# Optimization experiments

Hardware: AMD Instinct MI355X
Metric: run time of the kernel (lower is better)

Reference implementation:

```python
import jax, jax.numpy as jnp
import numpy as np

EPS = 1e-5

def _layernorm(x, gamma):
    # LayerNorm over last dim, no bias (torch LayerNorm(bias=False))
    mu = jnp.mean(x, axis=-1, keepdims=True)
    var = jnp.mean(jnp.square(x - mu), axis=-1, keepdims=True)
    return (x - mu) * jax.lax.rsqrt(var + EPS) * gamma

def setup_inputs() -> dict:
    B, N, D = 32, 1024, 512
    key = jax.random.key(0)
    ks = jax.random.split(key, 6)
    x = jax.random.normal(ks[0], (B, N, D), dtype=jnp.float32)
    # valid lengths in [1, N] so no query row has all keys masked
    belief_base_sizes = jax.random.randint(ks[1], (B,), 1, N + 1, dtype=jnp.int32)
    s = 0.02
    w_qkv = jax.random.normal(ks[2], (D, 3 * D), dtype=jnp.float32) * s
    w_fc = jax.random.normal(ks[3], (D, D), dtype=jnp.float32) * s
    w_proj = jax.random.normal(ks[4], (D, D), dtype=jnp.float32) * s
    g1 = jnp.ones((D,), dtype=jnp.float32)
    g2 = jnp.ones((D,), dtype=jnp.float32)
    return {"x": x, "belief_base_sizes": belief_base_sizes, "g1": g1,
            "w_qkv": w_qkv, "g2": g2, "w_fc": w_fc, "w_proj": w_proj}

def reference(x, belief_base_sizes, g1, w_qkv, g2, w_fc, w_proj):
    B, N, D = x.shape
    h = _layernorm(x, g1)                      # LN1
    qkv = jnp.einsum('bnd,de->bne', h, w_qkv)  # [B,N,3D]
    q, k, v = jnp.split(qkv, 3, axis=-1)
    scores = jnp.einsum('bqd,bkd->bqk', q, k) / jnp.sqrt(jnp.float32(D))
    # mask key columns >= valid size (rows are NOT masked, matching the original)
    col = jnp.arange(N)
    pad = col[None, None, :] >= belief_base_sizes[:, None, None]  # [B,1,N]
    scores = jnp.where(pad, -jnp.inf, scores)
    attn = jax.nn.softmax(scores, axis=-1)
    y = jnp.einsum('bqk,bkd->bqd', attn, v)
    y = _layernorm(y, g2)                      # LN2 (no residual in original)
    y = jnp.einsum('bnd,de->bne', y, w_fc)
    y = jax.nn.gelu(y, approximate=False)      # torch GELU default = exact erf
    y = jnp.einsum('bnd,de->bne', y, w_proj)
    return y
```

## Files before the change

kernel.cpp:

```cpp
#include <hip/hip_runtime.h>
#include <hip/hip_bf16.h>
#include <cmath>


using f16 = _Float16;
typedef _Float16 f16x8 __attribute__((ext_vector_type(8)));
typedef _Float16 f16x4 __attribute__((ext_vector_type(4)));
typedef _Float16 f16x2 __attribute__((ext_vector_type(2)));
typedef float f32x4 __attribute__((ext_vector_type(4)));

#define NB 32
#define NN 1024
#define ND 512

#define GLOAD_LDS16(g, l)                                                     \
    __builtin_amdgcn_global_load_lds(                                         \
        (const __attribute__((address_space(1))) void*)(g),                   \
        (__attribute__((address_space(3))) void*)(l), 16, 0, 0)

__global__ void transpose_cast_all(const float* __restrict__ wqkv, f16* __restrict__ wqkvT,
                                   const float* __restrict__ wfc, f16* __restrict__ wfcT,
                                   const float* __restrict__ wproj, f16* __restrict__ wprojT) {
    const int z = blockIdx.z;
    const float* w = (z == 0) ? wqkv : (z == 1) ? wfc : wproj;
    f16* wT       = (z == 0) ? wqkvT : (z == 1) ? wfcT : wprojT;
    const int Ncols = (z == 0) ? 1536 : 512;
    if ((int)blockIdx.x * 32 >= Ncols) return;

    __shared__ float tile[32][33];
    const int n0 = blockIdx.x * 32, k0 = blockIdx.y * 32;
    const int tx = threadIdx.x, ty = threadIdx.y;
    for (int i = ty; i < 32; i += 8)
        tile[i][tx] = w[(long long)(k0 + i) * Ncols + n0 + tx];
    __syncthreads();
    for (int i = ty; i < 32; i += 8)
        wT[(long long)(n0 + i) * 512 + k0 + tx] = (f16)tile[tx][i];
}

template <typename TIN>
__global__ __launch_bounds__(256) void ln_kernel(const TIN* __restrict__ x,
                                                 const float* __restrict__ gamma,
                                                 f16* __restrict__ out) {
    const int tid = threadIdx.x;
    const long long base = (long long)blockIdx.x * ND;
    float v0, v1;
    if constexpr (sizeof(TIN) == 4) {
        const float2 t = ((const float2*)(x + base))[tid];
        v0 = t.x; v1 = t.y;
    } else {
        const f16x2 t = ((const f16x2*)(x + base))[tid];
        v0 = (float)t.x; v1 = (float)t.y;
    }

    __shared__ float red[8];
    const int wave = tid >> 6, lane = tid & 63;

    float s = v0 + v1;
#pragma unroll
    for (int o = 32; o > 0; o >>= 1) s += __shfl_down(s, o, 64);
    if (lane == 0) red[wave] = s;
    __syncthreads();
    const float mean = (red[0] + red[1] + red[2] + red[3]) * (1.f / 512.f);
    __syncthreads();

    const float d0 = v0 - mean, d1 = v1 - mean;
    float q = d0 * d0 + d1 * d1;
#pragma unroll
    for (int o = 32; o > 0; o >>= 1) q += __shfl_down(q, o, 64);
    if (lane == 0) red[wave] = q;
    __syncthreads();
    const float var = (red[0] + red[1] + red[2] + red[3]) * (1.f / 512.f);
    const float rstd = rsqrtf(var + 1e-5f);

    f16x2 o2;
    o2.x = (f16)(d0 * rstd * gamma[2 * tid]);
    o2.y = (f16)(d1 * rstd * gamma[2 * tid + 1]);
    ((f16x2*)(out + base))[tid] = o2;
}

__global__ __launch_bounds__(256) void softmax_wave(f16* __restrict__ scores,
                                                    const int* __restrict__ sizes) {
    const int b = blockIdx.y;
    const int wave = threadIdx.x >> 6, lane = threadIdx.x & 63;
    const int row = blockIdx.x * 4 + wave;
    f16* srow = scores + ((long long)b * NN + row) * NN;
    const int sz = sizes[b];
    const int keff = (sz + 63) & ~63;
    const int cbase = lane * 16;

    const f16x8 a0 = *(const f16x8*)&srow[cbase];
    const f16x8 a1 = *(const f16x8*)&srow[cbase + 8];
    float v[16];
#pragma unroll
    for (int e = 0; e < 8; e++) { v[e] = (float)a0[e]; v[8 + e] = (float)a1[e]; }

    float m = -1e30f;
#pragma unroll
    for (int e = 0; e < 16; e++)
        if (cbase + e < sz) m = fmaxf(m, v[e]);
#pragma unroll
    for (int o = 32; o > 0; o >>= 1) m = fmaxf(m, __shfl_xor(m, o, 64));

    float s = 0.f;
#pragma unroll
    for (int e = 0; e < 16; e++) {
        v[e] = (cbase + e < sz) ? __expf(v[e] - m) : 0.f;
        s += v[e];
    }
#pragma unroll
    for (int o = 32; o > 0; o >>= 1) s += __shfl_xor(s, o, 64);
    const float inv = 1.f / s;

    if (cbase < keff) {
        f16x8 o0, o1;
#pragma unroll
        for (int e = 0; e < 8; e++) {
            o0[e] = (f16)(v[e] * inv);
            o1[e] = (f16)(v[8 + e] * inv);
        }
        *(f16x8*)&srow[cbase] = o0;
        *(f16x8*)&srow[cbase + 8] = o1;
    }
}

__device__ __forceinline__ float gelu_exact(float x) {
    return 0.5f * x * (1.f + erff(x * 0.70710678118654752f));
}

template <int MODE, int MASKN, int MASKK>
__global__ __launch_bounds__(256) void gemm_bt(
    const f16* __restrict__ A, int lda, long long strideA,
    const f16* __restrict__ Bt, int ldb, long long strideB,
    void* __restrict__ Cv, int ldc, long long strideC,
    int K, float alpha, const int* __restrict__ sizes, void* __restrict__ Cv2) {
    __shared__ __align__(16) f16 As[128 * 64];
    __shared__ __align__(16) f16 Bs[128 * 64];

    const int tid = threadIdx.x;
    const int wave = tid >> 6, lane = tid & 63;
    const int wr = (wave >> 1) * 64, wc = (wave & 1) * 64;
    const int lrow = lane & 15, quad = lane >> 4;
    const long long m0 = (long long)blockIdx.y * 128;
    const long long n0 = (long long)blockIdx.x * 128;

    if (MASKN) {
        if (n0 >= sizes[blockIdx.z]) return;
    }
    int Keff = K;
    if (MASKK) {
        const int ke = (sizes[blockIdx.z] + 63) & ~63;
        if (ke < Keff) Keff = ke;
    }

    A += (long long)blockIdx.z * strideA;
    Bt += (long long)blockIdx.z * strideB;

    f32x4 acc[4][4];
#pragma unroll
    for (int i = 0; i < 4; i++)
#pragma unroll
        for (int j = 0; j < 4; j++) acc[i][j] = (f32x4){0.f, 0.f, 0.f, 0.f};

    const f16* Ap[4];
    const f16* Bp[4];
#pragma unroll
    for (int p = 0; p < 4; p++) {
        const int s = tid + p * 256;
        const int r = s >> 3, c = ((s & 7) ^ (r & 7)) * 8;
        Ap[p] = A + (m0 + r) * lda + c;
        Bp[p] = Bt + (n0 + r) * ldb + c;
    }

    for (int k0 = 0; k0 < Keff; k0 += 64) {
        __syncthreads();
#pragma unroll
        for (int p = 0; p < 4; p++) GLOAD_LDS16(Ap[p] + k0, &As[(tid + p * 256) * 8]);
#pragma unroll
        for (int p = 0; p < 4; p++) GLOAD_LDS16(Bp[p] + k0, &Bs[(tid + p * 256) * 8]);
        __syncthreads();

#pragma unroll
        for (int h = 0; h < 2; h++) {
            const int gq = ((h * 4 + quad) ^ (lrow & 7)) * 8;
            f16x8 af[4], bf[4];
#pragma unroll
            for (int i = 0; i < 4; i++)
                af[i] = *(const f16x8*)&As[(wr + i * 16 + lrow) * 64 + gq];
#pragma unroll
            for (int j = 0; j < 4; j++)
                bf[j] = *(const f16x8*)&Bs[(wc + j * 16 + lrow) * 64 + gq];
#pragma unroll
            for (int i = 0; i < 4; i++)
#pragma unroll
                for (int j = 0; j < 4; j++)
                    acc[i][j] = __builtin_amdgcn_mfma_f32_16x16x32_f16(af[i], bf[j], acc[i][j], 0, 0, 0);
        }
    }

    if (MODE == 3 && n0 >= 1024) {
        f16* vTp = (f16*)Cv2;
#pragma unroll
        for (int i = 0; i < 4; i++) {
            const long long rbase = m0 + wr + i * 16 + quad * 4;
            const long long bb = rbase >> 10;
            const long long nrow = rbase & 1023;
#pragma unroll
            for (int j = 0; j < 4; j++) {
                const long long col = n0 + wc + j * 16 + lrow - 1024;
                f16x4 pk;
#pragma unroll
                for (int r = 0; r < 4; r++) pk[r] = (f16)acc[i][j][r];
                *(f16x4*)&vTp[bb * ND * NN + col * NN + nrow] = pk;
            }
        }
        return;
    }
    float* Cf = (float*)Cv + (long long)blockIdx.z * strideC;
    f16* Ch = (f16*)Cv + (long long)blockIdx.z * strideC;
#pragma unroll
    for (int i = 0; i < 4; i++) {
        const long long rbase = m0 + wr + i * 16 + quad * 4;
#pragma unroll
        for (int j = 0; j < 4; j++) {
            const long long col = n0 + wc + j * 16 + lrow;
#pragma unroll
            for (int r = 0; r < 4; r++) {
                float vv = acc[i][j][r];
                if (MODE == 1) {
                    Cf[(rbase + r) * ldc + col] = vv * alpha;
                } else if (MODE == 2) {
                    Ch[(rbase + r) * ldc + col] = (f16)gelu_exact(vv);
                } else {
                    Ch[(rbase + r) * ldc + col] = (f16)(vv * alpha);
                }
            }
        }
    }
}

extern "C" void kernel_launch(void* const* d_in, const int* in_sizes, int n_in,
                              void* d_out, int out_size, void* d_ws, size_t ws_size,
                              hipStream_t stream) {
    const float* x     = (const float*)d_in[0];
    const int*   sizes = (const int*)d_in[1];
    const float* g1    = (const float*)d_in[2];
    const float* wqkv  = (const float*)d_in[3];
    const float* g2    = (const float*)d_in[4];
    const float* wfc   = (const float*)d_in[5];
    const float* wproj = (const float*)d_in[6];
    float* out = (float*)d_out;
    char* ws = (char*)d_ws;

    f16* wqkvT  = (f16*)(ws + (0ull << 20));
    f16* wfcT   = (f16*)(ws + (2ull << 20));
    f16* wprojT = (f16*)(ws + (3ull << 20));
    f16* qk     = (f16*)(ws + (4ull << 20));
    f16* vT     = (f16*)(ws + (68ull << 20));
    f16* scoresB = (f16*)(ws + (4ull << 20));
    f16* ln2o   = (f16*)(ws + (36ull << 20));
    f16* gelub  = (f16*)(ws + (4ull << 20));

    f16* h       = (f16*)d_out;
    f16* scoresA = (f16*)d_out;
    f16* y       = (f16*)d_out + (long long)NB * NN * ND;

    const long long sstr = (long long)NN * NN;
    const long long qstr = (long long)NN * 1024;
    const long long vstr = (long long)ND * NN;
    const long long ystr = (long long)NN * ND;

    transpose_cast_all<<<dim3(48, 16, 3), dim3(32, 8), 0, stream>>>(
        wqkv, wqkvT, wfc, wfcT, wproj, wprojT);

    ln_kernel<float><<<NB * NN, 256, 0, stream>>>(x, g1, h);

    gemm_bt<3, 0, 0><<<dim3(12, 256, 1), 256, 0, stream>>>(
        h, 512, 0, wqkvT, 512, 0, qk, 1024, 0, 512, 1.0f, nullptr, vT);

    for (int ph = 0; ph < 2; ph++) {
        const int b0 = ph * 16;
        f16* sc = ph ? scoresB : scoresA;
        const f16* qc = qk + (long long)b0 * qstr;

        gemm_bt<0, 1, 0><<<dim3(8, 8, 16), 256, 0, stream>>>(
            qc, 1024, qstr, qc + 512, 1024, qstr,
            sc, NN, sstr, 512, 0.044194173824159216f, sizes + b0, nullptr);

        softmax_wave<<<dim3(NN / 4, 16), 256, 0, stream>>>(sc, sizes + b0);

        gemm_bt<0, 0, 1><<<dim3(4, 8, 16), 256, 0, stream>>>(
            sc, NN, sstr, vT + (long long)b0 * vstr, NN, vstr,
            y + (long long)b0 * ystr, ND, ystr, NN, 1.0f, sizes + b0, nullptr);
    }

    ln_kernel<f16><<<NB * NN, 256, 0, stream>>>(y, g2, ln2o);

    gemm_bt<2, 0, 0><<<dim3(4, 256, 1), 256, 0, stream>>>(
        ln2o, 512, 0, wfcT, 512, 0, gelub, 512, 0, 512, 1.0f, nullptr, nullptr);

    gemm_bt<1, 0, 0><<<dim3(4, 256, 1), 256, 0, stream>>>(
        gelub, 512, 0, wprojT, 512, 0, out, 512, 0, 512, 1.0f, nullptr, nullptr);
}
```

Measured before the change: 438.7 us.

## Merge attention phases into single launches, add XCD-aware tile remap, skip masked softmax loads

Buffers are relocated so the full-batch score matrix fits in the output buffer and y lives in the workspace. That lets the two half-batch attention phases collapse into one QK GEMM, one softmax and one PV GEMM over all 32 batches, cutting kernel launches and tail effects. Non-batched GEMMs remap block IDs so consecutive tiles land on the same XCD, aiming at better L2 reuse on MI355X. Softmax rows skip loading fp16 scores past the padded valid length. The buffer aliasing relies on qk no longer being needed once y is written over its start, and on vT being finished before gelub reuses its space.

```diff
diff --git a/kernel.cpp b/kernel.cpp
--- a/kernel.cpp
+++ b/kernel.cpp
@@ -88,11 +88,16 @@
     const int keff = (sz + 63) & ~63;
     const int cbase = lane * 16;
 
-    const f16x8 a0 = *(const f16x8*)&srow[cbase];
-    const f16x8 a1 = *(const f16x8*)&srow[cbase + 8];
     float v[16];
-#pragma unroll
-    for (int e = 0; e < 8; e++) { v[e] = (float)a0[e]; v[8 + e] = (float)a1[e]; }
+    if (cbase < keff) {
+        const f16x8 a0 = *(const f16x8*)&srow[cbase];
+        const f16x8 a1 = *(const f16x8*)&srow[cbase + 8];
+#pragma unroll
+        for (int e = 0; e < 8; e++) { v[e] = (float)a0[e]; v[8 + e] = (float)a1[e]; }
+    } else {
+#pragma unroll
+        for (int e = 0; e < 16; e++) v[e] = 0.f;
+    }
 
     float m = -1e30f;
 #pragma unroll
@@ -140,8 +145,21 @@
     const int wave = tid >> 6, lane = tid & 63;
     const int wr = (wave >> 1) * 64, wc = (wave & 1) * 64;
     const int lrow = lane & 15, quad = lane >> 4;
-    const long long m0 = (long long)blockIdx.y * 128;
-    const long long n0 = (long long)blockIdx.x * 128;
+
+    int bx = blockIdx.x, by = blockIdx.y;
+    if (gridDim.z == 1) {
+        const int gx = gridDim.x;
+        const int nwg = gx * (int)gridDim.y;
+        const int id = by * gx + bx;
+        const int q = nwg >> 3, r = nwg & 7;
+        const int xcd = id & 7, slot = id >> 3;
+        const int wid = (xcd < r) ? (xcd * (q + 1) + slot)
+                                  : (r * (q + 1) + (xcd - r) * q + slot);
+        bx = wid % gx;
+        by = wid / gx;
+    }
+    const long long m0 = (long long)by * 128;
+    const long long n0 = (long long)bx * 128;
 
     if (MASKN) {
         if (n0 >= sizes[blockIdx.z]) return;
@@ -256,13 +274,12 @@
     f16* wprojT = (f16*)(ws + (3ull << 20));
     f16* qk     = (f16*)(ws + (4ull << 20));
     f16* vT     = (f16*)(ws + (68ull << 20));
-    f16* scoresB = (f16*)(ws + (4ull << 20));
+    f16* y      = (f16*)(ws + (4ull << 20));
     f16* ln2o   = (f16*)(ws + (36ull << 20));
-    f16* gelub  = (f16*)(ws + (4ull << 20));
-
-    f16* h       = (f16*)d_out;
-    f16* scoresA = (f16*)d_out;
-    f16* y       = (f16*)d_out + (long long)NB * NN * ND;
+    f16* gelub  = (f16*)(ws + (68ull << 20));
+
+    f16* h      = (f16*)d_out;
+    f16* scores = (f16*)d_out;
 
     const long long sstr = (long long)NN * NN;
     const long long qstr = (long long)NN * 1024;
@@ -277,21 +294,15 @@
     gemm_bt<3, 0, 0><<<dim3(12, 256, 1), 256, 0, stream>>>(
         h, 512, 0, wqkvT, 512, 0, qk, 1024, 0, 512, 1.0f, nullptr, vT);
 
-    for (int ph = 0; ph < 2; ph++) {
-        const int b0 = ph * 16;
-        f16* sc = ph ? scoresB : scoresA;
-        const f16* qc = qk + (long long)b0 * qstr;
-
-        gemm_bt<0, 1, 0><<<dim3(8, 8, 16), 256, 0, stream>>>(
-            qc, 1024, qstr, qc + 512, 1024, qstr,
-            sc, NN, sstr, 512, 0.044194173824159216f, sizes + b0, nullptr);
-
-        softmax_wave<<<dim3(NN / 4, 16), 256, 0, stream>>>(sc, sizes + b0);
-
-        gemm_bt<0, 0, 1><<<dim3(4, 8, 16), 256, 0, stream>>>(
-            sc, NN, sstr, vT + (long long)b0 * vstr, NN, vstr,
-            y + (long long)b0 * ystr, ND, ystr, NN, 1.0f, sizes + b0, nullptr);
-    }
+    gemm_bt<0, 1, 0><<<dim3(8, 8, 32), 256, 0, stream>>>(
+        qk, 1024, qstr, qk + 512, 1024, qstr,
+        scores, NN, sstr, 512, 0.044194173824159216f, sizes, nullptr);
+
+    softmax_wave<<<dim3(NN / 4, NB), 256, 0, stream>>>(scores, sizes);
+
+    gemm_bt<0, 0, 1><<<dim3(4, 8, 32), 256, 0, stream>>>(
+        scores, NN, sstr, vT, NN, vstr,
+        y, ND, ystr, NN, 1.0f, sizes, nullptr);
 
     ln_kernel<f16><<<NB * NN, 256, 0, stream>>>(y, g2, ln2o);
 
```

New measurement: 409.0 us. 1.07x faster.
